# Kernel tuning notes

Hardware: AMD Instinct MI355X
Metric: run time of the kernel (lower is better)

## Reference

```python
import jax, jax.numpy as jnp
import numpy as np


def setup_inputs() -> dict:
    key = jax.random.key(0)
    k1, k2 = jax.random.split(key)
    B, S, D, E = 4, 8192, 1024, 64
    x = jax.random.normal(k1, (B, S, D), dtype=jnp.float32)
    W = jax.random.normal(k2, (E, D), dtype=jnp.float32) * (1.0 / np.sqrt(D))
    return {"x": x, "W": W, "top_k": 1}


EXPERT_CAPACITY = 640


def reference(x, W, top_k):
    # Router logits: small-dim linear (bias=False), jitter=0 so no noise.
    logits = jnp.einsum("bsd,ed->bse", x, W)              # [B,S,E]
    probs = jax.nn.softmax(logits, axis=-1)               # [B,S,E]
    num_experts = W.shape[0]
    # top-k over experts (top_k == 1 here)
    top_k_values, top_k_indices = jax.lax.top_k(probs, top_k)  # [B,S,k]
    # one-hot over experts, summed over the k slots -> [B,S,E] int mask
    expert_indices = jax.nn.one_hot(top_k_indices, num_experts, dtype=jnp.int32).sum(axis=-2)
    # token priority: running count of tokens assigned to each expert along seq
    token_priority = jnp.cumsum(expert_indices, axis=-2)  # [B,S,E]
    capacity_mask = token_priority <= EXPERT_CAPACITY
    expert_indices = expert_indices * capacity_mask.astype(jnp.int32)
    # top_k_values [B,S,1] broadcasts over E (valid only for k==1, as in torch)
    router_probs = top_k_values * expert_indices.astype(top_k_values.dtype)
    return expert_indices, router_probs, logits
```

## Files before the change

kernel.cpp:

```cpp
#include <hip/hip_runtime.h>
#include <hip/hip_bf16.h>

#define NB 4
#define NS 8192
#define ND 1024
#define NE 64
#define NM (NB * NS)
#define CAPACITY 640

#define BM 64
#define BK 64
#define NKT (ND / BK)
#define NCHUNK (NM / BM)
#define CPB (NS / BM)

typedef short short8 __attribute__((ext_vector_type(8)));
typedef unsigned short ushort8 __attribute__((ext_vector_type(8)));
typedef float f32x4 __attribute__((ext_vector_type(4)));

__device__ __forceinline__ int swz(int row, int colshorts) {
    return row * 64 + (colshorts ^ ((row & 7) << 3));
}

__global__ __launch_bounds__(256) void w_conv(const float* __restrict__ W,
                                              unsigned short* __restrict__ Wh,
                                              unsigned short* __restrict__ Wl)
{
    const int i = (blockIdx.x * 256 + threadIdx.x) * 4;
    float4 v = *(const float4*)(W + i);
    float f[4] = {v.x, v.y, v.z, v.w};
    ushort4 h, l;
    unsigned short* hp = &h.x;
    unsigned short* lp = &l.x;
#pragma unroll
    for (int c = 0; c < 4; ++c) {
        __hip_bfloat16 hb = __float2bfloat16(f[c]);
        float r = f[c] - __bfloat162float(hb);
        __hip_bfloat16 lb = __float2bfloat16(r);
        hp[c] = __builtin_bit_cast(unsigned short, hb);
        lp[c] = __builtin_bit_cast(unsigned short, lb);
    }
    *(ushort4*)(Wh + i) = h;
    *(ushort4*)(Wl + i) = l;
}

__global__ __launch_bounds__(256) void k1_mfma(const float* __restrict__ x,
                                               const unsigned short* __restrict__ Wh,
                                               const unsigned short* __restrict__ Wl,
                                               float* __restrict__ logits,
                                               float* __restrict__ e_out,
                                               float* __restrict__ p_out,
                                               int* __restrict__ idx_ws,
                                               float* __restrict__ prob_ws,
                                               int* __restrict__ hist)
{
    __shared__ short xs_h[64 * 64];
    __shared__ short xs_l[64 * 64];
    __shared__ short whs[64 * 64];
    __shared__ short wls[64 * 64];
    __shared__ int lh[NE];

    const int tid = threadIdx.x;
    const int lane = tid & 63;
    const int wv = tid >> 6;
    const int lr = lane & 15;
    const int kq = lane >> 4;
    const int tok0 = blockIdx.x * BM;
    const int wtok = tok0 + wv * 16;

    if (tid < NE) lh[tid] = 0;

    {
        const float4 z = {0.f, 0.f, 0.f, 0.f};
        size_t b0 = (size_t)tok0 * NE;
#pragma unroll
        for (int i = 0; i < 4; ++i) {
            *(float4*)&e_out[b0 + (size_t)(i * 256 + tid) * 4] = z;
            *(float4*)&p_out[b0 + (size_t)(i * 256 + tid) * 4] = z;
        }
    }

    const int xrow = tid >> 2;
    const int xcol = (tid & 3) * 16;
    const float* xsrc = x + (size_t)(tok0 + xrow) * ND + xcol;

    const int we0 = tid >> 3;
    const int wcol = (tid & 7) * 8;

    f32x4 acc[4];
#pragma unroll
    for (int j = 0; j < 4; ++j) acc[j] = (f32x4){0.f, 0.f, 0.f, 0.f};

    float4 px[4], px2[4];
#pragma unroll
    for (int c = 0; c < 4; ++c) px[c] = *(const float4*)(xsrc + c * 4);

    for (int kt = 0; kt < NKT; ++kt) {
        const int k0 = kt * BK;
        if (kt > 0) __syncthreads();

#pragma unroll
        for (int i = 0; i < 2; ++i) {
            const int e = we0 + i * 32;
            const size_t gs = (size_t)e * ND + k0 + wcol;
            ushort8 vh = *(const ushort8*)(Wh + gs);
            ushort8 vl = *(const ushort8*)(Wl + gs);
            *(ushort8*)&whs[swz(e, wcol)] = vh;
            *(ushort8*)&wls[swz(e, wcol)] = vl;
        }

#pragma unroll
        for (int c = 0; c < 4; ++c) {
            float f[4] = {px[c].x, px[c].y, px[c].z, px[c].w};
            ushort4 h4, l4;
            unsigned short* hp = &h4.x;
            unsigned short* lp = &l4.x;
#pragma unroll
            for (int e = 0; e < 4; ++e) {
                unsigned int u = __builtin_bit_cast(unsigned int, f[e]);
                hp[e] = (unsigned short)(u >> 16);
                float fhi = __builtin_bit_cast(float, u & 0xFFFF0000u);
                lp[e] = (unsigned short)(__builtin_bit_cast(unsigned int, f[e] - fhi) >> 16);
            }
            const int si = swz(xrow, xcol + c * 4);
            *(ushort4*)&xs_h[si] = h4;
            *(ushort4*)&xs_l[si] = l4;
        }

        if (kt + 1 < NKT) {
#pragma unroll
            for (int c = 0; c < 4; ++c)
                px2[c] = *(const float4*)(xsrc + (k0 + BK) + c * 4);
        }

        __syncthreads();

#pragma unroll
        for (int kk = 0; kk < 2; ++kk) {
            const int col = kk * 32 + kq * 8;
            const int arow = wv * 16 + lr;
            short8 ah = *(const short8*)&xs_h[swz(arow, col)];
            short8 al = *(const short8*)&xs_l[swz(arow, col)];
#pragma unroll
            for (int j = 0; j < 4; ++j) {
                const int erow = j * 16 + lr;
                short8 bh = *(const short8*)&whs[swz(erow, col)];
                short8 bl = *(const short8*)&wls[swz(erow, col)];
                acc[j] = __builtin_amdgcn_mfma_f32_16x16x32_bf16(ah, bh, acc[j], 0, 0, 0);
                acc[j] = __builtin_amdgcn_mfma_f32_16x16x32_bf16(ah, bl, acc[j], 0, 0, 0);
                acc[j] = __builtin_amdgcn_mfma_f32_16x16x32_bf16(al, bh, acc[j], 0, 0, 0);
            }
        }

#pragma unroll
        for (int c = 0; c < 4; ++c) px[c] = px2[c];
    }

#pragma unroll
    for (int r = 0; r < 4; ++r) {
        const int t = wtok + kq * 4 + r;
        float val[4];
#pragma unroll
        for (int j = 0; j < 4; ++j) val[j] = acc[j][r];

        float m = val[0];
        int mi = lr;
#pragma unroll
        for (int j = 1; j < 4; ++j) {
            if (val[j] > m) { m = val[j]; mi = j * 16 + lr; }
        }
#pragma unroll
        for (int off = 1; off < 16; off <<= 1) {
            float m2 = __shfl_xor(m, off);
            int mi2 = __shfl_xor(mi, off);
            if (m2 > m || (m2 == m && mi2 < mi)) { m = m2; mi = mi2; }
        }
        float s = 0.0f;
#pragma unroll
        for (int j = 0; j < 4; ++j) s += __expf(val[j] - m);
#pragma unroll
        for (int off = 1; off < 16; off <<= 1) s += __shfl_xor(s, off);

#pragma unroll
        for (int j = 0; j < 4; ++j) {
            logits[(size_t)t * NE + j * 16 + lr] = val[j];
        }
        if (lr == 0) {
            idx_ws[t] = mi;
            prob_ws[t] = 1.0f / s;
            atomicAdd(&lh[mi], 1);
        }
    }
    __syncthreads();
    if (tid < NE) hist[blockIdx.x * NE + tid] = lh[tid];
}

__global__ __launch_bounds__(256) void k_scan(const int* __restrict__ hist,
                                              int* __restrict__ base)
{
    const int b = threadIdx.x >> 6;
    const int e = threadIdx.x & 63;
    int run = 0;
#pragma unroll 8
    for (int c = 0; c < CPB; ++c) {
        int idx = (b * CPB + c) * NE + e;
        base[idx] = run;
        run += hist[idx];
    }
}

__global__ __launch_bounds__(64) void k_scatter(const int* __restrict__ idx_ws,
                                                const float* __restrict__ prob_ws,
                                                const int* __restrict__ base,
                                                float* __restrict__ e_out,
                                                float* __restrict__ p_out)
{
    __shared__ int sIdx[BM];
    __shared__ float sProb[BM];
    const int c = blockIdx.x;
    const int lane = threadIdx.x;
    const int t0 = c * BM;
    sIdx[lane] = idx_ws[t0 + lane];
    sProb[lane] = prob_ws[t0 + lane];
    __syncthreads();

    int counter = base[c * NE + lane];
    for (int j = 0; j < BM; ++j) {
        if (sIdx[j] == lane) {
            ++counter;
            if (counter <= CAPACITY) {
                size_t g = (size_t)(t0 + j) * NE + lane;
                e_out[g] = 1.0f;
                p_out[g] = sProb[j];
            }
        }
    }
}

extern "C" void kernel_launch(void* const* d_in, const int* in_sizes, int n_in,
                              void* d_out, int out_size, void* d_ws, size_t ws_size,
                              hipStream_t stream)
{
    const float* x = (const float*)d_in[0];
    const float* W = (const float*)d_in[1];

    float* out = (float*)d_out;
    float* e_out = out;
    float* p_out = out + (size_t)NM * NE;
    float* logits = out + 2 * (size_t)NM * NE;

    char* ws = (char*)d_ws;
    int* idx_ws    = (int*)ws;
    float* prob_ws = (float*)(ws + (size_t)NM * 4);
    int* hist      = (int*)(ws + (size_t)NM * 8);
    int* base      = (int*)(ws + (size_t)NM * 8 + (size_t)NCHUNK * NE * 4);
    unsigned short* Wh = (unsigned short*)(ws + (size_t)NM * 8 + (size_t)NCHUNK * NE * 8);
    unsigned short* Wl = Wh + (size_t)NE * ND;

    w_conv<<<NE * ND / (256 * 4), 256, 0, stream>>>(W, Wh, Wl);
    k1_mfma<<<NM / BM, 256, 0, stream>>>(x, Wh, Wl, logits, e_out, p_out,
                                         idx_ws, prob_ws, hist);
    k_scan<<<1, 256, 0, stream>>>(hist, base);
    k_scatter<<<NCHUNK, 64, 0, stream>>>(idx_ws, prob_ws, base, e_out, p_out);
}
```

Measured before the change: 55.09 us.

## Fuse scan and scatter into the GEMM kernel via cooperative grid sync

The separate scan and scatter kernels are replaced by a cooperative launch of the main MFMA kernel. After a grid-wide sync, each block computes its per-expert prefix from the histogram and writes dense e_out and p_out tiles exactly once. The earlier zero-fill plus sparse scatter goes away, and so do the idx/prob workspace round-trips. Logits are staged through LDS (reusing the x tile buffer) so global stores are coalesced float4 writes. The cost is a grid barrier and a requirement that all 512 blocks be co-resident (launch_bounds 256,2); if they cannot be, the cooperative launch fails.

```diff
diff --git a/kernel.cpp b/kernel.cpp
--- a/kernel.cpp
+++ b/kernel.cpp
@@ -1,5 +1,8 @@
 #include <hip/hip_runtime.h>
 #include <hip/hip_bf16.h>
+#include <hip/hip_cooperative_groups.h>
+
+namespace cg = cooperative_groups;
 
 #define NB 4
 #define NS 8192
@@ -11,7 +14,7 @@
 #define BM 64
 #define BK 64
 #define NKT (ND / BK)
-#define NCHUNK (NM / BM)
+#define NBLK (NM / BM)
 #define CPB (NS / BM)
 
 typedef short short8 __attribute__((ext_vector_type(8)));
@@ -44,21 +47,26 @@
     *(ushort4*)(Wl + i) = l;
 }
 
-__global__ __launch_bounds__(256) void k1_mfma(const float* __restrict__ x,
-                                               const unsigned short* __restrict__ Wh,
-                                               const unsigned short* __restrict__ Wl,
-                                               float* __restrict__ logits,
-                                               float* __restrict__ e_out,
-                                               float* __restrict__ p_out,
-                                               int* __restrict__ idx_ws,
-                                               float* __restrict__ prob_ws,
-                                               int* __restrict__ hist)
+__global__ __launch_bounds__(256, 2) void k1_mfma(const float* __restrict__ x,
+                                                  const unsigned short* __restrict__ Wh,
+                                                  const unsigned short* __restrict__ Wl,
+                                                  float* __restrict__ logits,
+                                                  float* __restrict__ e_out,
+                                                  float* __restrict__ p_out,
+                                                  int* __restrict__ hist)
 {
-    __shared__ short xs_h[64 * 64];
-    __shared__ short xs_l[64 * 64];
+    __shared__ char sbuf[16384];
     __shared__ short whs[64 * 64];
     __shared__ short wls[64 * 64];
     __shared__ int lh[NE];
+    __shared__ int sMi[BM];
+    __shared__ float sPr[BM];
+    __shared__ int sAd[BM];
+    __shared__ int pp[4][NE];
+
+    short* xs_h = (short*)sbuf;
+    short* xs_l = (short*)(sbuf + 8192);
+    float* sLog = (float*)sbuf;
 
     const int tid = threadIdx.x;
     const int lane = tid & 63;
@@ -66,19 +74,8 @@
     const int lr = lane & 15;
     const int kq = lane >> 4;
     const int tok0 = blockIdx.x * BM;
-    const int wtok = tok0 + wv * 16;
 
     if (tid < NE) lh[tid] = 0;
-
-    {
-        const float4 z = {0.f, 0.f, 0.f, 0.f};
-        size_t b0 = (size_t)tok0 * NE;
-#pragma unroll
-        for (int i = 0; i < 4; ++i) {
-            *(float4*)&e_out[b0 + (size_t)(i * 256 + tid) * 4] = z;
-            *(float4*)&p_out[b0 + (size_t)(i * 256 + tid) * 4] = z;
-        }
-    }
 
     const int xrow = tid >> 2;
     const int xcol = (tid & 3) * 16;
@@ -156,9 +153,11 @@
         for (int c = 0; c < 4; ++c) px[c] = px2[c];
     }
 
+    __syncthreads();
+
 #pragma unroll
     for (int r = 0; r < 4; ++r) {
-        const int t = wtok + kq * 4 + r;
+        const int tl = wv * 16 + kq * 4 + r;
         float val[4];
 #pragma unroll
         for (int j = 0; j < 4; ++j) val[j] = acc[j][r];
@@ -182,58 +181,63 @@
         for (int off = 1; off < 16; off <<= 1) s += __shfl_xor(s, off);
 
 #pragma unroll
-        for (int j = 0; j < 4; ++j) {
-            logits[(size_t)t * NE + j * 16 + lr] = val[j];
-        }
+        for (int j = 0; j < 4; ++j) sLog[tl * NE + j * 16 + lr] = val[j];
         if (lr == 0) {
-            idx_ws[t] = mi;
-            prob_ws[t] = 1.0f / s;
+            sMi[tl] = mi;
+            sPr[tl] = 1.0f / s;
             atomicAdd(&lh[mi], 1);
         }
     }
     __syncthreads();
+
+    const size_t g0 = (size_t)tok0 * NE;
+#pragma unroll
+    for (int i = 0; i < 4; ++i) {
+        const int fl = i * 1024 + tid * 4;
+        *(float4*)&logits[g0 + fl] = *(const float4*)&sLog[fl];
+    }
     if (tid < NE) hist[blockIdx.x * NE + tid] = lh[tid];
-}
-
-__global__ __launch_bounds__(256) void k_scan(const int* __restrict__ hist,
-                                              int* __restrict__ base)
-{
-    const int b = threadIdx.x >> 6;
-    const int e = threadIdx.x & 63;
-    int run = 0;
-#pragma unroll 8
-    for (int c = 0; c < CPB; ++c) {
-        int idx = (b * CPB + c) * NE + e;
-        base[idx] = run;
-        run += hist[idx];
-    }
-}
-
-__global__ __launch_bounds__(64) void k_scatter(const int* __restrict__ idx_ws,
-                                                const float* __restrict__ prob_ws,
-                                                const int* __restrict__ base,
-                                                float* __restrict__ e_out,
-                                                float* __restrict__ p_out)
-{
-    __shared__ int sIdx[BM];
-    __shared__ float sProb[BM];
-    const int c = blockIdx.x;
-    const int lane = threadIdx.x;
-    const int t0 = c * BM;
-    sIdx[lane] = idx_ws[t0 + lane];
-    sProb[lane] = prob_ws[t0 + lane];
-    __syncthreads();
-
-    int counter = base[c * NE + lane];
-    for (int j = 0; j < BM; ++j) {
-        if (sIdx[j] == lane) {
-            ++counter;
-            if (counter <= CAPACITY) {
-                size_t g = (size_t)(t0 + j) * NE + lane;
-                e_out[g] = 1.0f;
-                p_out[g] = sProb[j];
-            }
-        }
+
+    cg::this_grid().sync();
+
+    const int b = blockIdx.x / CPB;
+    const int cin = blockIdx.x % CPB;
+
+    {
+        int run = 0;
+        const int* hrow = hist + (size_t)b * CPB * NE + lane;
+        for (int c = wv; c < cin; c += 4) run += hrow[c * NE];
+        pp[wv][lane] = run;
+    }
+    __syncthreads();
+
+    if (wv == 0) {
+        int run = pp[0][lane] + pp[1][lane] + pp[2][lane] + pp[3][lane];
+        for (int j = 0; j < BM; ++j) {
+            if (sMi[j] == lane) { ++run; sAd[j] = (run <= CAPACITY) ? 1 : 0; }
+        }
+    }
+    __syncthreads();
+
+#pragma unroll
+    for (int i = 0; i < 4; ++i) {
+        const int fl = i * 1024 + tid * 4;
+        const int t = fl >> 6;
+        const int e0 = fl & 63;
+        const int mi = sMi[t];
+        const float pr = sPr[t];
+        const int ad = sAd[t];
+        float4 ev, pv;
+        float* evp = &ev.x;
+        float* pvp = &pv.x;
+#pragma unroll
+        for (int c = 0; c < 4; ++c) {
+            const bool hit = (mi == e0 + c) && ad;
+            evp[c] = hit ? 1.0f : 0.0f;
+            pvp[c] = hit ? pr : 0.0f;
+        }
+        *(float4*)&e_out[g0 + fl] = ev;
+        *(float4*)&p_out[g0 + fl] = pv;
     }
 }
 
@@ -250,16 +254,21 @@
     float* logits = out + 2 * (size_t)NM * NE;
 
     char* ws = (char*)d_ws;
-    int* idx_ws    = (int*)ws;
-    float* prob_ws = (float*)(ws + (size_t)NM * 4);
-    int* hist      = (int*)(ws + (size_t)NM * 8);
-    int* base      = (int*)(ws + (size_t)NM * 8 + (size_t)NCHUNK * NE * 4);
-    unsigned short* Wh = (unsigned short*)(ws + (size_t)NM * 8 + (size_t)NCHUNK * NE * 8);
-    unsigned short* Wl = Wh + (size_t)NE * ND;
+    int* hist = (int*)ws;
+    unsigned short* Wh = (unsigned short*)(ws + 131072);
+    unsigned short* Wl = (unsigned short*)(ws + 262144);
 
     w_conv<<<NE * ND / (256 * 4), 256, 0, stream>>>(W, Wh, Wl);
-    k1_mfma<<<NM / BM, 256, 0, stream>>>(x, Wh, Wl, logits, e_out, p_out,
-                                         idx_ws, prob_ws, hist);
-    k_scan<<<1, 256, 0, stream>>>(hist, base);
-    k_scatter<<<NCHUNK, 64, 0, stream>>>(idx_ws, prob_ws, base, e_out, p_out);
-}
+
+    const float* xa = x;
+    const unsigned short* wha = Wh;
+    const unsigned short* wla = Wl;
+    float* la = logits;
+    float* ea = e_out;
+    float* pa = p_out;
+    int* ha = hist;
+    void* kargs[] = {(void*)&xa, (void*)&wha, (void*)&wla, (void*)&la,
+                     (void*)&ea, (void*)&pa, (void*)&ha};
+    hipLaunchCooperativeKernel((const void*)k1_mfma, dim3(NBLK), dim3(256),
+                               kargs, 0, stream);
+}
```

Result: slower. 100.3 us (+82.0%).
